# Performance work log

Hardware: AMD Instinct MI355X
Metric: run time of the kernel (lower is better)

Reference implementation:

```python
import jax, jax.numpy as jnp
import numpy as np

NEG_SLOPE = 0.01  # F.leaky_relu default in GATLayer.edge_attention
N_NODES = 50000
N_EDGES = 1600000
IN_DIM = 128
HEADS = 8
D_HEAD = 16  # out_dim / head_num = 128 / 8


def setup_inputs() -> dict:
    key = jax.random.key(0)
    ks = jax.random.split(key, 9)
    # glorot-ish scales for linear projections and attention vectors
    w_scale = (2.0 / (IN_DIM + D_HEAD)) ** 0.5
    a_scale = (2.0 / (2 * D_HEAD + 1)) ** 0.5
    return {
        "x": jax.random.normal(ks[0], (N_NODES, IN_DIM), dtype=jnp.float32),
        "src": jax.random.randint(ks[1], (N_EDGES,), 0, N_NODES, dtype=jnp.int32),
        "dst": jax.random.randint(ks[2], (N_EDGES,), 0, N_NODES, dtype=jnp.int32),
        "W1": jax.random.normal(ks[3], (HEADS, IN_DIM, D_HEAD), dtype=jnp.float32) * w_scale,
        "a1_src": jax.random.normal(ks[4], (HEADS, D_HEAD), dtype=jnp.float32) * a_scale,
        "a1_dst": jax.random.normal(ks[5], (HEADS, D_HEAD), dtype=jnp.float32) * a_scale,
        "W2": jax.random.normal(ks[6], (HEADS, IN_DIM, D_HEAD), dtype=jnp.float32) * w_scale,
        "a2_src": jax.random.normal(ks[7], (HEADS, D_HEAD), dtype=jnp.float32) * a_scale,
        "a2_dst": jax.random.normal(ks[8], (HEADS, D_HEAD), dtype=jnp.float32) * a_scale,
    }


def gat_multihead(h, src, dst, W, a_src, a_dst, num_nodes):
    """One MultiHeadLayer(GATLayer) with concat merge. h: [N, Din]."""
    z = jnp.einsum("nd,hdk->nhk", h, W)            # [N,H,Dh] per-head projection
    # attn_fc(cat(z_src, z_dst)) == a_src . z_src + a_dst . z_dst
    s_src = jnp.einsum("nhk,hk->nh", z, a_src)      # [N,H]
    s_dst = jnp.einsum("nhk,hk->nh", z, a_dst)      # [N,H]
    e = jax.nn.leaky_relu(s_src[src] + s_dst[dst], NEG_SLOPE)  # [E,H]
    # segment softmax over incoming edges of each dst node
    e_max = jax.ops.segment_max(e, dst, num_segments=num_nodes)          # [N,H]
    e_max = jnp.where(jnp.isfinite(e_max), e_max, 0.0)                   # empty segments
    w = jnp.exp(e - e_max[dst])                                          # [E,H]
    denom = jax.ops.segment_sum(w, dst, num_segments=num_nodes)          # [N,H]
    msg = w[:, :, None] * z[src]                                         # [E,H,Dh]
    num = jax.ops.segment_sum(msg, dst, num_segments=num_nodes)          # [N,H,Dh]
    out = num / jnp.where(denom == 0.0, 1.0, denom)[:, :, None]
    return out.reshape(num_nodes, -1)                                    # concat heads -> [N, H*Dh]


def reference(x, src, dst, W1, a1_src, a1_dst, W2, a2_src, a2_dst):
    n = x.shape[0]
    h = gat_multihead(x, src, dst, W1, a1_src, a1_dst, n)
    h = jax.nn.elu(h)
    h = gat_multihead(h, src, dst, W2, a2_src, a2_dst, n)
    return h
```

## Files before the change

kernel.cpp:

```cpp
#include <hip/hip_runtime.h>
#include <hip/hip_bf16.h>

#define N_NODES 50000
#define N_EDGES 1600000
#define NEG_SLOPE 0.01f
#define WPAD 136

#define NBKT 256
#define BKTW 196
#define NBLK1 200
#define CHUNK1 8000

typedef _Float16 v8h __attribute__((ext_vector_type(8)));
typedef _Float16 v2h __attribute__((ext_vector_type(2)));
typedef float v4f __attribute__((ext_vector_type(4)));

__global__ __launch_bounds__(256) void proj_mfma_kernel(
    const float* __restrict__ x,
    const float* __restrict__ W,
    _Float16* __restrict__ z)
{
    __shared__ _Float16 Wl[128 * WPAD];

    const int t = threadIdx.x;
    for (int i = t; i < 16384; i += 256) {
        const int h = i >> 11, k = (i >> 4) & 127, col = i & 15;
        Wl[(h * 16 + col) * WPAD + k] = (_Float16)W[i];
    }
    __syncthreads();

    const int wid = t >> 6;
    const int l   = t & 63;
    const int lc  = l & 15;
    const int kg  = l >> 4;

    const int nwaves = gridDim.x * 4;
    for (int tile = blockIdx.x * 4 + wid; tile < N_NODES / 16; tile += nwaves) {
        const int n0 = tile * 16;
        v4f acc[8];
#pragma unroll
        for (int ht = 0; ht < 8; ht++) acc[ht] = (v4f)0.f;

#pragma unroll
        for (int kb = 0; kb < 4; kb++) {
            const float4* xp = (const float4*)&x[(n0 + lc) * 128 + kb * 32 + kg * 8];
            const float4 xa = xp[0];
            const float4 xb = xp[1];
            v8h a;
            a[0] = (_Float16)xa.x; a[1] = (_Float16)xa.y;
            a[2] = (_Float16)xa.z; a[3] = (_Float16)xa.w;
            a[4] = (_Float16)xb.x; a[5] = (_Float16)xb.y;
            a[6] = (_Float16)xb.z; a[7] = (_Float16)xb.w;
#pragma unroll
            for (int ht = 0; ht < 8; ht++) {
                const v8h b = *(const v8h*)&Wl[(ht * 16 + lc) * WPAD + kb * 32 + kg * 8];
                acc[ht] = __builtin_amdgcn_mfma_f32_16x16x32_f16(a, b, acc[ht], 0, 0, 0);
            }
        }

        _Float16* zp = &z[(n0 + 4 * kg) * 128 + lc];
#pragma unroll
        for (int ht = 0; ht < 8; ht++)
#pragma unroll
            for (int i = 0; i < 4; i++)
                zp[i * 128 + ht * 16] = (_Float16)acc[ht][i];
    }
}

__global__ __launch_bounds__(256) void score_kernel(
    const _Float16* __restrict__ z,
    const float* __restrict__ a_src, const float* __restrict__ a_dst,
    float* __restrict__ s_src, float* __restrict__ s_dst)
{
    __shared__ float asl[128], adl[128];
    const int t = threadIdx.x;
    if (t < 128) { asl[t] = a_src[t]; adl[t] = a_dst[t]; }
    __syncthreads();

    const int idx = blockIdx.x * 256 + t;
    if (idx >= N_NODES * 8) return;
    const int n = idx >> 3, h = idx & 7;

    const v8h z0 = *(const v8h*)&z[n * 128 + h * 16];
    const v8h z1 = *(const v8h*)&z[n * 128 + h * 16 + 8];
    float ss = 0.f, sd = 0.f;
#pragma unroll
    for (int j = 0; j < 8; j++) {
        ss = fmaf((float)z0[j], asl[h * 16 + j], ss);
        sd = fmaf((float)z0[j], adl[h * 16 + j], sd);
    }
#pragma unroll
    for (int j = 0; j < 8; j++) {
        ss = fmaf((float)z1[j], asl[h * 16 + 8 + j], ss);
        sd = fmaf((float)z1[j], adl[h * 16 + 8 + j], sd);
    }
    s_src[idx] = ss;
    s_dst[idx] = sd;
}

__global__ __launch_bounds__(256) void hist_bucket_kernel(
    const int* __restrict__ dst, int* __restrict__ bh)
{
    __shared__ int lhist[NBKT];
    const int t = threadIdx.x, blk = blockIdx.x;
    lhist[t] = 0;
    __syncthreads();
    const int e0 = blk * CHUNK1, e1 = e0 + CHUNK1;
    for (int e = e0 + t; e < e1; e += 256)
        atomicAdd(&lhist[(unsigned)dst[e] / BKTW], 1);
    __syncthreads();
    bh[t * NBLK1 + blk] = lhist[t];
}

__global__ __launch_bounds__(256) void scan_buckets_kernel(
    int* __restrict__ bh, int* __restrict__ btotal)
{
    __shared__ int sb[256];
    const int t = threadIdx.x, b = blockIdx.x;
    const int v = (t < NBLK1) ? bh[b * NBLK1 + t] : 0;
    sb[t] = v;
    __syncthreads();
    int x = v;
    for (int off = 1; off < 256; off <<= 1) {
        const int add = (t >= off) ? sb[t - off] : 0;
        __syncthreads();
        x += add;
        sb[t] = x;
        __syncthreads();
    }
    if (t < NBLK1) bh[b * NBLK1 + t] = x - v;
    if (t == 255) btotal[b] = x;
}

__global__ __launch_bounds__(256) void scan_totals_kernel(
    const int* __restrict__ btotal, int* __restrict__ bstart)
{
    __shared__ int sb[256];
    const int t = threadIdx.x;
    const int v = btotal[t];
    sb[t] = v;
    __syncthreads();
    int x = v;
    for (int off = 1; off < 256; off <<= 1) {
        const int add = (t >= off) ? sb[t - off] : 0;
        __syncthreads();
        x += add;
        sb[t] = x;
        __syncthreads();
    }
    bstart[t] = x - v;
    if (t == 255) bstart[256] = x;
}

__global__ __launch_bounds__(256) void scatter_bucket_kernel(
    const int* __restrict__ src, const int* __restrict__ dst,
    const int* __restrict__ bh, const int* __restrict__ bstart,
    int* __restrict__ gbuf)
{
    __shared__ int lbase[NBKT];
    __shared__ int lcur[NBKT];
    const int t = threadIdx.x, blk = blockIdx.x;
    lbase[t] = bstart[t] + bh[t * NBLK1 + blk];
    lcur[t] = 0;
    __syncthreads();
    const int e0 = blk * CHUNK1, e1 = e0 + CHUNK1;
    for (int e = e0 + t; e < e1; e += 256) {
        const int d = dst[e];
        const unsigned b = (unsigned)d / BKTW;
        const int ld = d - (int)b * BKTW;
        const int r = atomicAdd(&lcur[b], 1);
        gbuf[lbase[b] + r] = (ld << 16) | src[e];
    }
}

__global__ __launch_bounds__(256) void sort_bucket_kernel(
    const int* __restrict__ gbuf, const int* __restrict__ bstart,
    int* __restrict__ perm, int* __restrict__ rowp)
{
    __shared__ int lhist[NBKT];
    __shared__ int lscan[NBKT];
    __shared__ int lcur[NBKT];
    const int t = threadIdx.x, b = blockIdx.x;
    const int base = bstart[b];
    const int cnt  = bstart[b + 1] - base;
    const int n0   = b * BKTW;

    lhist[t] = 0;
    lcur[t] = 0;
    __syncthreads();
    for (int i = t; i < cnt; i += 256)
        atomicAdd(&lhist[gbuf[base + i] >> 16], 1);
    __syncthreads();

    const int v = lhist[t];
    lscan[t] = v;
    __syncthreads();
    int x = v;
    for (int off = 1; off < 256; off <<= 1) {
        const int add = (t >= off) ? lscan[t - off] : 0;
        __syncthreads();
        x += add;
        lscan[t] = x;
        __syncthreads();
    }
    const int excl = x - v;
    __syncthreads();
    lscan[t] = excl;

    const int n = n0 + t;
    if (t < BKTW && n < N_NODES) rowp[n] = base + excl;
    if (b == NBKT - 1 && t == 0) rowp[N_NODES] = bstart[NBKT];
    __syncthreads();

    for (int i = t; i < cnt; i += 256) {
        const int e = gbuf[base + i];
        const int ld = e >> 16;
        const int r = atomicAdd(&lcur[ld], 1);
        perm[base + lscan[ld] + r] = e & 0xFFFF;
    }
}

__global__ __launch_bounds__(256) void edge_weight_kernel(
    const int* __restrict__ rowp, const int* __restrict__ perm,
    const float* __restrict__ s_src, const float* __restrict__ s_dst,
    __hip_bfloat16* __restrict__ wperm)
{
    const int wv = threadIdx.x >> 6;
    const int l  = threadIdx.x & 63;
    const int n  = blockIdx.x * 4 + wv;

    const int e8 = l >> 3;
    const int h8 = l & 7;

    const int start = rowp[n];
    const int end   = rowp[n + 1];
    const float sd  = s_dst[n * 8 + h8];

    for (int j0 = start; j0 < end; j0 += 8) {
        const int jj = j0 + e8;
        if (jj < end) {
            const int se = perm[jj];
            float s = s_src[se * 8 + h8] + sd;
            s = s > 0.f ? s : NEG_SLOPE * s;
            wperm[jj * 8 + h8] = __float2bfloat16(__expf(s));
        }
    }
}

__global__ __launch_bounds__(256) void gather_kernel(
    const int* __restrict__ row_ptr, const int* __restrict__ perm,
    const __hip_bfloat16* __restrict__ wperm,
    const _Float16* __restrict__ z,
    float* __restrict__ out, const int apply_elu)
{
    const int wv = threadIdx.x >> 6;
    const int l  = threadIdx.x & 63;
    const int n  = blockIdx.x * 4 + wv;

    const int c0 = 2 * l;
    const int h  = l >> 3;

    const int start = row_ptr[n];
    const int end   = row_ptr[n + 1];

    float acc0 = 0.f, acc1 = 0.f, wsum = 0.f;

    for (int j0 = start; j0 < end; j0 += 8) {
#pragma unroll
        for (int k = 0; k < 8; k++) {
            const int jr = j0 + k;
            const int jj = (jr < end) ? jr : end - 1;
            const int se = perm[jj];
            float w = __bfloat162float(wperm[jj * 8 + h]);
            w = (jr < end) ? w : 0.f;
            const v2h zv = *(const v2h*)&z[se * 128 + c0];
            wsum += w;
            acc0 = fmaf(w, (float)zv[0], acc0);
            acc1 = fmaf(w, (float)zv[1], acc1);
        }
    }

    const float inv = (end > start) ? 1.f / wsum : 0.f;
    float o0 = acc0 * inv;
    float o1 = acc1 * inv;
    if (apply_elu) {
        o0 = o0 > 0.f ? o0 : expm1f(o0);
        o1 = o1 > 0.f ? o1 : expm1f(o1);
    }
    *(float2*)&out[n * 128 + c0] = make_float2(o0, o1);
}

extern "C" void kernel_launch(void* const* d_in, const int* in_sizes, int n_in,
                              void* d_out, int out_size, void* d_ws, size_t ws_size,
                              hipStream_t stream) {
    const float* x    = (const float*)d_in[0];
    const int*   src  = (const int*)d_in[1];
    const int*   dst  = (const int*)d_in[2];
    const float* W1   = (const float*)d_in[3];
    const float* a1s  = (const float*)d_in[4];
    const float* a1d  = (const float*)d_in[5];
    const float* W2   = (const float*)d_in[6];
    const float* a2s  = (const float*)d_in[7];
    const float* a2d  = (const float*)d_in[8];
    float* out = (float*)d_out;

    char* p = (char*)d_ws;
    _Float16* z  = (_Float16*)p;  p += (size_t)N_NODES * 128 * 2;
    __hip_bfloat16* wperm = (__hip_bfloat16*)p; p += (size_t)N_EDGES * 8 * 2;
    float* ssrc  = (float*)p;     p += (size_t)N_NODES * 8 * 4;
    float* sdst  = (float*)p;     p += (size_t)N_NODES * 8 * 4;
    int*   rowp  = (int*)p;       p += ((size_t)N_NODES + 4) * 4;
    int*   bh    = (int*)p;       p += (size_t)NBKT * NBLK1 * 4;
    int*   btot  = (int*)p;       p += (size_t)NBKT * 4;
    int*   bstart= (int*)p;       p += ((size_t)NBKT + 4) * 4;
    int*   gbuf  = (int*)p;       p += (size_t)N_EDGES * 4;
    int*   perm  = (int*)p;       p += (size_t)N_EDGES * 4;

    const int PROJ_GRID   = 391;
    const int SCORE_GRID  = (N_NODES * 8 + 255) / 256;
    const int NODE4_GRID  = N_NODES / 4;

    hist_bucket_kernel<<<NBLK1, 256, 0, stream>>>(dst, bh);
    scan_buckets_kernel<<<NBKT, 256, 0, stream>>>(bh, btot);
    scan_totals_kernel<<<1, 256, 0, stream>>>(btot, bstart);
    scatter_bucket_kernel<<<NBLK1, 256, 0, stream>>>(src, dst, bh, bstart, gbuf);
    sort_bucket_kernel<<<NBKT, 256, 0, stream>>>(gbuf, bstart, perm, rowp);

    proj_mfma_kernel<<<PROJ_GRID, 256, 0, stream>>>(x, W1, z);
    score_kernel<<<SCORE_GRID, 256, 0, stream>>>(z, a1s, a1d, ssrc, sdst);
    edge_weight_kernel<<<NODE4_GRID, 256, 0, stream>>>(rowp, perm, ssrc, sdst, wperm);
    gather_kernel<<<NODE4_GRID, 256, 0, stream>>>(rowp, perm, wperm, z, out, 1);

    proj_mfma_kernel<<<PROJ_GRID, 256, 0, stream>>>(out, W2, z);
    score_kernel<<<SCORE_GRID, 256, 0, stream>>>(z, a2s, a2d, ssrc, sdst);
    edge_weight_kernel<<<NODE4_GRID, 256, 0, stream>>>(rowp, perm, ssrc, sdst, wperm);
    gather_kernel<<<NODE4_GRID, 256, 0, stream>>>(rowp, perm, wperm, z, out, 0);
}
```

Before: 256.6 us.

## Fuse edge-weight computation into gather kernel using wave shuffles

```diff
diff --git a/kernel.cpp b/kernel.cpp
--- a/kernel.cpp
+++ b/kernel.cpp
@@ -216,14 +216,16 @@
         const int e = gbuf[base + i];
         const int ld = e >> 16;
         const int r = atomicAdd(&lcur[ld], 1);
-        perm[base + lscan[ld] + r] = e & 0xFFFF;
-    }
-}
-
-__global__ __launch_bounds__(256) void edge_weight_kernel(
-    const int* __restrict__ rowp, const int* __restrict__ perm,
-    const float* __restrict__ s_src, const float* __restrict__ s_dst,
-    __hip_bfloat16* __restrict__ wperm)
+        perm[base + lscan[ld] + r] = (e & 0xFFFF) << 8;
+    }
+}
+
+__global__ __launch_bounds__(256) void gather_kernel(
+    const int* __restrict__ row_ptr, const int* __restrict__ perm,
+    const char* __restrict__ zb,
+    const char* __restrict__ ssb,
+    const float* __restrict__ s_dst,
+    float* __restrict__ out, const int apply_elu)
 {
     const int wv = threadIdx.x >> 6;
     const int l  = threadIdx.x & 63;
@@ -231,52 +233,34 @@
 
     const int e8 = l >> 3;
     const int h8 = l & 7;
-
-    const int start = rowp[n];
-    const int end   = rowp[n + 1];
-    const float sd  = s_dst[n * 8 + h8];
-
-    for (int j0 = start; j0 < end; j0 += 8) {
-        const int jj = j0 + e8;
-        if (jj < end) {
-            const int se = perm[jj];
-            float s = s_src[se * 8 + h8] + sd;
-            s = s > 0.f ? s : NEG_SLOPE * s;
-            wperm[jj * 8 + h8] = __float2bfloat16(__expf(s));
-        }
-    }
-}
-
-__global__ __launch_bounds__(256) void gather_kernel(
-    const int* __restrict__ row_ptr, const int* __restrict__ perm,
-    const __hip_bfloat16* __restrict__ wperm,
-    const _Float16* __restrict__ z,
-    float* __restrict__ out, const int apply_elu)
-{
-    const int wv = threadIdx.x >> 6;
-    const int l  = threadIdx.x & 63;
-    const int n  = blockIdx.x * 4 + wv;
-
-    const int c0 = 2 * l;
     const int h  = l >> 3;
 
     const int start = row_ptr[n];
     const int end   = row_ptr[n + 1];
+    const float sd8 = s_dst[n * 8 + h8];
 
     float acc0 = 0.f, acc1 = 0.f, wsum = 0.f;
 
     for (int j0 = start; j0 < end; j0 += 8) {
+        const int off = perm[j0 + e8];
+        float s = *(const float*)(ssb + (off >> 3) + h8 * 4) + sd8;
+        s = s > 0.f ? s : NEG_SLOPE * s;
+        float w = __expf(s);
+        w = (j0 + e8 < end) ? w : 0.f;
+
+        int offk[8];
+#pragma unroll
+        for (int k = 0; k < 8; k++) offk[k] = __shfl(off, k * 8 + h);
+        v2h zv[8];
+#pragma unroll
+        for (int k = 0; k < 8; k++)
+            zv[k] = *(const v2h*)(zb + offk[k] + 4 * l);
 #pragma unroll
         for (int k = 0; k < 8; k++) {
-            const int jr = j0 + k;
-            const int jj = (jr < end) ? jr : end - 1;
-            const int se = perm[jj];
-            float w = __bfloat162float(wperm[jj * 8 + h]);
-            w = (jr < end) ? w : 0.f;
-            const v2h zv = *(const v2h*)&z[se * 128 + c0];
-            wsum += w;
-            acc0 = fmaf(w, (float)zv[0], acc0);
-            acc1 = fmaf(w, (float)zv[1], acc1);
+            const float wk = __shfl(w, k * 8 + h);
+            wsum += wk;
+            acc0 = fmaf(wk, (float)zv[k][0], acc0);
+            acc1 = fmaf(wk, (float)zv[k][1], acc1);
         }
     }
 
@@ -287,7 +271,7 @@
         o0 = o0 > 0.f ? o0 : expm1f(o0);
         o1 = o1 > 0.f ? o1 : expm1f(o1);
     }
-    *(float2*)&out[n * 128 + c0] = make_float2(o0, o1);
+    *(float2*)&out[n * 128 + 2 * l] = make_float2(o0, o1);
 }
 
 extern "C" void kernel_launch(void* const* d_in, const int* in_sizes, int n_in,
@@ -306,7 +290,6 @@
 
     char* p = (char*)d_ws;
     _Float16* z  = (_Float16*)p;  p += (size_t)N_NODES * 128 * 2;
-    __hip_bfloat16* wperm = (__hip_bfloat16*)p; p += (size_t)N_EDGES * 8 * 2;
     float* ssrc  = (float*)p;     p += (size_t)N_NODES * 8 * 4;
     float* sdst  = (float*)p;     p += (size_t)N_NODES * 8 * 4;
     int*   rowp  = (int*)p;       p += ((size_t)N_NODES + 4) * 4;
@@ -314,12 +297,13 @@
     int*   btot  = (int*)p;       p += (size_t)NBKT * 4;
     int*   bstart= (int*)p;       p += ((size_t)NBKT + 4) * 4;
     int*   gbuf  = (int*)p;       p += (size_t)N_EDGES * 4;
-    int*   perm  = (int*)p;       p += (size_t)N_EDGES * 4;
+    int*   perm  = (int*)p;       p += ((size_t)N_EDGES + 8) * 4;
 
     const int PROJ_GRID   = 391;
     const int SCORE_GRID  = (N_NODES * 8 + 255) / 256;
     const int NODE4_GRID  = N_NODES / 4;
 
+    hipMemsetAsync(perm + N_EDGES, 0, 8 * 4, stream);
     hist_bucket_kernel<<<NBLK1, 256, 0, stream>>>(dst, bh);
     scan_buckets_kernel<<<NBKT, 256, 0, stream>>>(bh, btot);
     scan_totals_kernel<<<1, 256, 0, stream>>>(btot, bstart);
@@ -328,11 +312,11 @@
 
     proj_mfma_kernel<<<PROJ_GRID, 256, 0, stream>>>(x, W1, z);
     score_kernel<<<SCORE_GRID, 256, 0, stream>>>(z, a1s, a1d, ssrc, sdst);
-    edge_weight_kernel<<<NODE4_GRID, 256, 0, stream>>>(rowp, perm, ssrc, sdst, wperm);
-    gather_kernel<<<NODE4_GRID, 256, 0, stream>>>(rowp, perm, wperm, z, out, 1);
+    gather_kernel<<<NODE4_GRID, 256, 0, stream>>>(rowp, perm, (const char*)z,
+                                                  (const char*)ssrc, sdst, out, 1);
 
     proj_mfma_kernel<<<PROJ_GRID, 256, 0, stream>>>(out, W2, z);
     score_kernel<<<SCORE_GRID, 256, 0, stream>>>(z, a2s, a2d, ssrc, sdst);
-    edge_weight_kernel<<<NODE4_GRID, 256, 0, stream>>>(rowp, perm, ssrc, sdst, wperm);
-    gather_kernel<<<NODE4_GRID, 256, 0, stream>>>(rowp, perm, wperm, z, out, 0);
-}
+    gather_kernel<<<NODE4_GRID, 256, 0, stream>>>(rowp, perm, (const char*)z,
+                                                  (const char*)ssrc, sdst, out, 0);
+}
```

New measurement: 228.3 us. -11.0%, faster.
